# Kernel optimization log

Hardware: AMD Instinct MI355X
Metric: run time of the kernel (lower is better)

Reference implementation:

```python
import jax, jax.numpy as jnp
import numpy as np

IN_DIM = 4096
OUT_DIM = 2048
K = 4
R = 4096
B = 4096


def setup_inputs() -> dict:
    key = jax.random.key(0)
    ks = jax.random.split(key, 8)
    s = 0.02
    return {
        "hidden_states": jax.random.normal(ks[0], (B, IN_DIM), jnp.float32),
        # stacked per-block weights, torch Linear layout: W1/W3 [k+1, out, in], W2 [k+1, in, out]
        "W1": jax.random.normal(ks[1], (K + 1, OUT_DIM, IN_DIM), jnp.float32) * s,
        "W3": jax.random.normal(ks[2], (K + 1, OUT_DIM, IN_DIM), jnp.float32) * s,
        "W2": jax.random.normal(ks[3], (K + 1, IN_DIM, OUT_DIM), jnp.float32) * s,
        "fc1_w": jax.random.normal(ks[4], (R, IN_DIM * K), jnp.float32) * s,
        "fc1_b": jax.random.normal(ks[5], (R,), jnp.float32) * s,
        "fc2_w": jax.random.normal(ks[6], (IN_DIM, R), jnp.float32) * s,
        "fc2_b": jax.random.normal(ks[7], (IN_DIM,), jnp.float32) * s,
    }


def reference(hidden_states, W1, W3, W2, fc1_w, fc1_b, fc2_w, fc2_b):
    x = hidden_states
    # batched SwiGLU over k+1 blocks: [B, k+1, out]
    g = jax.nn.silu(jnp.einsum("bi,koi->bko", x, W1)) * jnp.einsum("bi,koi->bko", x, W3)
    wk_outs = jnp.einsum("bko,kio->bki", g, W2)  # [B, k+1, in]
    o0 = wk_outs[:, 0]                            # [B, in]
    concat = wk_outs[:, 1:].reshape(x.shape[0], -1)  # [B, k*in], matches torch.cat order
    h = jax.nn.silu(concat @ fc1_w.T + fc1_b)
    proj = h @ fc2_w.T + fc2_b                    # [B, in]
    diff = o0 - proj
    return (jnp.linalg.norm(diff, ord=2, axis=1), jnp.mean(jnp.abs(diff), axis=1))
```

## Files before the change

### kernel.cpp

```cpp
#include <hip/hip_runtime.h>
#include <hip/hip_bf16.h>
#include <cstdint>
#include <cstddef>

#define IN_DIM 4096
#define OUT_DIM 2048
#define NEXP 5
#define KEXP 4
#define RDIM 4096
#define BATCH 4096

typedef __hip_bfloat16 bf16;
typedef __attribute__((ext_vector_type(8))) short bf16x8;
typedef __attribute__((ext_vector_type(4))) float f32x4;
typedef __attribute__((ext_vector_type(8))) unsigned short u16x8;
typedef __attribute__((ext_vector_type(4))) unsigned short u16x4;

typedef const __attribute__((address_space(1))) unsigned int* as1p;
typedef __attribute__((address_space(3))) unsigned int* as3p;

__device__ __forceinline__ unsigned short f2bf(float x) {
  union { __hip_bfloat16 h; unsigned short u; } cv;
  cv.h = __float2bfloat16(x);
  return cv.u;
}

__global__ __launch_bounds__(256) void cvt_kernel(const float* __restrict__ in,
                                                  unsigned short* __restrict__ out,
                                                  int n8) {
  int i = blockIdx.x * 256 + threadIdx.x;
  if (i >= n8) return;
  const float4* p = (const float4*)in;
  float4 a = p[(size_t)i * 2];
  float4 b = p[(size_t)i * 2 + 1];
  u16x8 v;
  v[0] = f2bf(a.x); v[1] = f2bf(a.y); v[2] = f2bf(a.z); v[3] = f2bf(a.w);
  v[4] = f2bf(b.x); v[5] = f2bf(b.y); v[6] = f2bf(b.z); v[7] = f2bf(b.w);
  *(u16x8*)(out + (size_t)i * 8) = v;
}

__global__ __launch_bounds__(256) void tcvt_kernel(const float* __restrict__ in,
                                                   unsigned short* __restrict__ out,
                                                   int NI, int NO) {
  __shared__ float tile[32][33];
  const float* inz = in + (size_t)blockIdx.z * NI * NO;
  unsigned short* outz = out + (size_t)blockIdx.z * NI * NO;
  int i0 = blockIdx.y * 32;
  int o0 = blockIdx.x * 32;
  int t = threadIdx.x;
  int ri = t >> 3, ro = (t & 7) << 2;
  float4 v = *(const float4*)(inz + (size_t)(i0 + ri) * NO + o0 + ro);
  tile[ri][ro] = v.x; tile[ri][ro + 1] = v.y; tile[ri][ro + 2] = v.z; tile[ri][ro + 3] = v.w;
  __syncthreads();
  int wo = t >> 3, wi = (t & 7) << 2;
  u16x4 w;
  w[0] = f2bf(tile[wi][wo]);
  w[1] = f2bf(tile[wi + 1][wo]);
  w[2] = f2bf(tile[wi + 2][wo]);
  w[3] = f2bf(tile[wi + 3][wo]);
  *(u16x4*)(outz + (size_t)(o0 + wo) * NI + i0 + wi) = w;
}

__device__ __forceinline__ void gload16(const bf16* g, bf16* l) {
  __builtin_amdgcn_global_load_lds((as1p)g, (as3p)l, 16, 0, 0);
}

template <int N> __device__ __forceinline__ void vwait() {
  if constexpr (N == 0) asm volatile("s_waitcnt vmcnt(0)" ::: "memory");
  else if constexpr (N == 2) asm volatile("s_waitcnt vmcnt(2)" ::: "memory");
  else if constexpr (N == 4) asm volatile("s_waitcnt vmcnt(4)" ::: "memory");
}

#define READ_A(buf, mh)                                              \
  do {                                                               \
    const bf16* _pa = ldsA + (buf) * 16384 + (mh) * 8192;            \
    _Pragma("unroll") for (int m2 = 0; m2 < 4; ++m2) {               \
      afr[m2][0] = *(const bf16x8*)(_pa + aOff[m2]);                 \
      afr[m2][1] = *(const bf16x8*)(_pa + (aOff[m2] ^ 32));          \
    }                                                                \
  } while (0)

#define READ_B(buf, nh)                                              \
  do {                                                               \
    const bf16* _pb = ldsB + (buf) * 16384 + (nh) * 8192;            \
    _Pragma("unroll") for (int n2 = 0; n2 < 2; ++n2) {               \
      bfr[(nh) * 2 + n2][0] = *(const bf16x8*)(_pb + bOff[(nh) * 2 + n2]);        \
      bfr[(nh) * 2 + n2][1] = *(const bf16x8*)(_pb + (bOff[(nh) * 2 + n2] ^ 32)); \
    }                                                                \
  } while (0)

#define QMFMA(mh, nh)                                                            \
  do {                                                                           \
    __builtin_amdgcn_s_setprio(1);                                               \
    _Pragma("unroll") for (int m2 = 0; m2 < 4; ++m2) {                           \
      _Pragma("unroll") for (int n2 = 0; n2 < 2; ++n2) {                         \
        acc[(mh) * 4 + m2][(nh) * 2 + n2] = __builtin_amdgcn_mfma_f32_16x16x32_bf16( \
            afr[m2][0], bfr[(nh) * 2 + n2][0], acc[(mh) * 4 + m2][(nh) * 2 + n2], 0, 0, 0); \
        acc[(mh) * 4 + m2][(nh) * 2 + n2] = __builtin_amdgcn_mfma_f32_16x16x32_bf16( \
            afr[m2][1], bfr[(nh) * 2 + n2][1], acc[(mh) * 4 + m2][(nh) * 2 + n2], 0, 0, 0); \
      }                                                                          \
    }                                                                            \
    __builtin_amdgcn_s_setprio(0);                                               \
  } while (0)

#define BAR() __builtin_amdgcn_s_barrier()

template <int EPI>
__global__ __launch_bounds__(512, 2) void gemm8p(
    const bf16* __restrict__ A, int lda, long long aZ,
    const bf16* __restrict__ B, int ldb, long long bZ,
    int Kdim,
    unsigned short* __restrict__ C, int ldc, long long cZ,
    const float* __restrict__ bias,
    const bf16* __restrict__ AUX, int ldaux, long long auxZ,
    float* __restrict__ accum,
    int gx, int gxy, int nwg8) {
  extern __shared__ __align__(16) bf16 lds[];
  bf16* ldsA = lds;
  bf16* ldsB = lds + 32768;

  int flat = blockIdx.x;
  int wg = (flat & 7) * nwg8 + (flat >> 3);
  int z = wg / gxy;
  int r0 = wg - z * gxy;
  int by = r0 / gx;
  int bx = r0 - by * gx;
  int rowBase = by * 256, colBase = bx * 256;

  int tid = threadIdx.x;
  int wave = tid >> 6, lane = tid & 63;
  int wr = wave >> 2, wc = wave & 3;

  const bf16* Ab = A + (long long)z * aZ + (long long)rowBase * lda;
  const bf16* Bb = B + (long long)z * bZ + (long long)colBase * ldb;

  int rl = tid >> 3;
  int cg8 = ((tid & 7) ^ (rl & 7)) << 3;
  int srcA = rl * lda + cg8;
  int srcB = rl * ldb + cg8;
  int dstOfs = wave * 512;

  int aOff[4], bOff[4];
#pragma unroll
  for (int m2 = 0; m2 < 4; ++m2) {
    int rA = ((2 * m2 + wr) * 16) + (lane & 15);
    aOff[m2] = rA * 64 + (((lane >> 4) ^ (rA & 7)) << 3);
  }
#pragma unroll
  for (int n = 0; n < 4; ++n) {
    int rB = (((4 * n + wc) * 16) & 127) + (lane & 15);
    bOff[n] = rB * 64 + (((lane >> 4) ^ (rB & 7)) << 3);
  }

  f32x4 acc[8][4] = {};
  bf16x8 afr[4][2], bfr[4][2];

  auto stA = [&](int buf, int hh, int kt) {
    const bf16* s = Ab + (long long)(hh * 128) * lda + kt * 64;
    bf16* d = ldsA + buf * 16384 + hh * 8192 + dstOfs;
    gload16(s + srcA, d);
    gload16(s + srcA + 64 * lda, d + 4096);
  };
  auto stB = [&](int buf, int hh, int kt) {
    const bf16* s = Bb + (long long)(hh * 128) * ldb + kt * 64;
    bf16* d = ldsB + buf * 16384 + hh * 8192 + dstOfs;
    gload16(s + srcB, d);
    gload16(s + srcB + 64 * ldb, d + 4096);
  };

  int NT = Kdim >> 6;
  int cur = 0;

  stA(0, 0, 0); stB(0, 0, 0); stB(0, 1, 0); stA(0, 1, 0);
  vwait<4>();
  BAR();

  for (int t = 0; t < NT - 1; ++t) {
    int nb = cur ^ 1;
    READ_A(cur, 0);
    READ_B(cur, 0);
    stA(nb, 0, t + 1);
    vwait<4>();
    BAR();
    QMFMA(0, 0);
    READ_B(cur, 1);
    stB(nb, 0, t + 1);
    vwait<4>();
    BAR();
    QMFMA(0, 1);
    READ_A(cur, 1);
    stB(nb, 1, t + 1);
    BAR();
    QMFMA(1, 1);
    stA(nb, 1, t + 1);
    vwait<4>();
    BAR();
    QMFMA(1, 0);
    cur = nb;
  }

  READ_A(cur, 0);
  READ_B(cur, 0);
  vwait<2>();
  BAR();
  QMFMA(0, 0);
  READ_B(cur, 1);
  vwait<0>();
  BAR();
  QMFMA(0, 1);
  READ_A(cur, 1);
  QMFMA(1, 1);
  QMFMA(1, 0);

  if constexpr (EPI == 2) {
    const bf16* AUXb = AUX + (long long)z * auxZ;
#pragma unroll
    for (int m = 0; m < 8; ++m) {
#pragma unroll
      for (int r = 0; r < 4; ++r) {
        int row = rowBase + (2 * m + wr) * 16 + ((lane >> 4) << 2) + r;
        float ssq = 0.f, sab = 0.f;
#pragma unroll
        for (int n = 0; n < 4; ++n) {
          int col = colBase + (4 * n + wc) * 16 + (lane & 15);
          float p = acc[m][n][r] + bias[col];
          float d = __bfloat162float(AUXb[(long long)row * ldaux + col]) - p;
          ssq += d * d;
          sab += fabsf(d);
        }
#pragma unroll
        for (int off = 1; off < 16; off <<= 1) {
          ssq += __shfl_xor(ssq, off);
          sab += __shfl_xor(sab, off);
        }
        if ((lane & 15) == 0) {
          atomicAdd(&accum[row], ssq);
          atomicAdd(&accum[BATCH + row], sab);
        }
      }
    }
  } else {
    unsigned short* Cb = C + (long long)z * cZ;
    const bf16* AUXb = (EPI == 3) ? (AUX + (long long)z * auxZ) : nullptr;
#pragma unroll
    for (int m = 0; m < 8; ++m) {
#pragma unroll
      for (int n = 0; n < 4; ++n) {
        int col = colBase + (4 * n + wc) * 16 + (lane & 15);
#pragma unroll
        for (int r = 0; r < 4; ++r) {
          int row = rowBase + (2 * m + wr) * 16 + ((lane >> 4) << 2) + r;
          float v = acc[m][n][r];
          if constexpr (EPI == 1) {
            v += bias[col];
            v = v / (1.f + __expf(-v));
          } else if constexpr (EPI == 3) {
            float s = __bfloat162float(AUXb[(long long)row * ldaux + col]);
            v = v * (s / (1.f + __expf(-s)));
          }
          Cb[(long long)row * ldc + col] = f2bf(v);
        }
      }
    }
  }
}

#define READ_B1(buf)                                                  \
  do {                                                                \
    const bf16* _pb = ldsB1 + (buf) * 8192;                           \
    _Pragma("unroll") for (int n2 = 0; n2 < 2; ++n2) {                \
      b1fr[n2][0] = *(const bf16x8*)(_pb + bOff[n2]);                 \
      b1fr[n2][1] = *(const bf16x8*)(_pb + (bOff[n2] ^ 32));          \
    }                                                                 \
  } while (0)

#define READ_B3(buf)                                                  \
  do {                                                                \
    const bf16* _pb = ldsB3 + (buf) * 8192;                           \
    _Pragma("unroll") for (int n2 = 0; n2 < 2; ++n2) {                \
      b3fr[n2][0] = *(const bf16x8*)(_pb + bOff[n2]);                 \
      b3fr[n2][1] = *(const bf16x8*)(_pb + (bOff[n2] ^ 32));          \
    }                                                                 \
  } while (0)

#define QMFMA_D(ACC, mh, BF)                                                     \
  do {                                                                           \
    __builtin_amdgcn_s_setprio(1);                                               \
    _Pragma("unroll") for (int m2 = 0; m2 < 4; ++m2) {                           \
      _Pragma("unroll") for (int n2 = 0; n2 < 2; ++n2) {                         \
        ACC[(mh) * 4 + m2][n2] = __builtin_amdgcn_mfma_f32_16x16x32_bf16(        \
            afr[m2][0], BF[n2][0], ACC[(mh) * 4 + m2][n2], 0, 0, 0);             \
        ACC[(mh) * 4 + m2][n2] = __builtin_amdgcn_mfma_f32_16x16x32_bf16(        \
            afr[m2][1], BF[n2][1], ACC[(mh) * 4 + m2][n2], 0, 0, 0);             \
      }                                                                          \
    }                                                                            \
    __builtin_amdgcn_s_setprio(0);                                               \
  } while (0)

__global__ __launch_bounds__(512, 2) void gemm_dual(
    const bf16* __restrict__ A,
    const bf16* __restrict__ W1b, const bf16* __restrict__ W3b,
    unsigned short* __restrict__ G,
    int gx, int gxy, int nwg8) {
  extern __shared__ __align__(16) bf16 lds[];
  bf16* ldsA = lds;
  bf16* ldsB1 = lds + 32768;
  bf16* ldsB3 = lds + 49152;

  int flat = blockIdx.x;
  int wg = (flat & 7) * nwg8 + (flat >> 3);
  int z = wg / gxy;
  int r0 = wg - z * gxy;
  int by = r0 / gx;
  int bx = r0 - by * gx;
  int rowBase = by * 256, colBase = bx * 128;

  int tid = threadIdx.x;
  int wave = tid >> 6, lane = tid & 63;
  int wr = wave >> 2, wc = wave & 3;

  const bf16* Ab = A + (long long)rowBase * IN_DIM;
  const bf16* B1b = W1b + (long long)z * OUT_DIM * IN_DIM + (long long)colBase * IN_DIM;
  const bf16* B3b = W3b + (long long)z * OUT_DIM * IN_DIM + (long long)colBase * IN_DIM;

  int rl = tid >> 3;
  int cg8 = ((tid & 7) ^ (rl & 7)) << 3;
  int src = rl * IN_DIM + cg8;
  int dstOfs = wave * 512;

  int aOff[4], bOff[2];
#pragma unroll
  for (int m2 = 0; m2 < 4; ++m2) {
    int rA = ((2 * m2 + wr) * 16) + (lane & 15);
    aOff[m2] = rA * 64 + (((lane >> 4) ^ (rA & 7)) << 3);
  }
#pragma unroll
  for (int n2 = 0; n2 < 2; ++n2) {
    int rB = (4 * n2 + wc) * 16 + (lane & 15);
    bOff[n2] = rB * 64 + (((lane >> 4) ^ (rB & 7)) << 3);
  }

  f32x4 acc1[8][2] = {};
  f32x4 acc2[8][2] = {};
  bf16x8 afr[4][2], b1fr[2][2], b3fr[2][2];

  auto stA = [&](int buf, int hh, int kt) {
    const bf16* s = Ab + (long long)(hh * 128) * IN_DIM + kt * 64;
    bf16* d = ldsA + buf * 16384 + hh * 8192 + dstOfs;
    gload16(s + src, d);
    gload16(s + src + 64 * IN_DIM, d + 4096);
  };
  auto stB1 = [&](int buf, int kt) {
    const bf16* s = B1b + kt * 64;
    bf16* d = ldsB1 + buf * 8192 + dstOfs;
    gload16(s + src, d);
    gload16(s + src + 64 * IN_DIM, d + 4096);
  };
  auto stB3 = [&](int buf, int kt) {
    const bf16* s = B3b + kt * 64;
    bf16* d = ldsB3 + buf * 8192 + dstOfs;
    gload16(s + src, d);
    gload16(s + src + 64 * IN_DIM, d + 4096);
  };

  const int NT = IN_DIM >> 6;
  int cur = 0;

  stA(0, 0, 0); stB1(0, 0); stB3(0, 0); stA(0, 1, 0);
  vwait<4>();
  BAR();

  for (int t = 0; t < NT - 1; ++t) {
    int nb = cur ^ 1;
    READ_A(cur, 0);
    READ_B1(cur);
    stA(nb, 0, t + 1);
    vwait<4>();
    BAR();
    QMFMA_D(acc1, 0, b1fr);
    READ_B3(cur);
    stB1(nb, t + 1);
    vwait<4>();
    BAR();
    QMFMA_D(acc2, 0, b3fr);
    READ_A(cur, 1);
    stB3(nb, t + 1);
    BAR();
    QMFMA_D(acc1, 1, b1fr);
    stA(nb, 1, t + 1);
    vwait<4>();
    BAR();
    QMFMA_D(acc2, 1, b3fr);
    cur = nb;
  }

  READ_A(cur, 0);
  READ_B1(cur);
  vwait<2>();
  BAR();
  QMFMA_D(acc1, 0, b1fr);
  READ_B3(cur);
  vwait<0>();
  BAR();
  QMFMA_D(acc2, 0, b3fr);
  READ_A(cur, 1);
  QMFMA_D(acc1, 1, b1fr);
  QMFMA_D(acc2, 1, b3fr);

  unsigned short* Gb = G + (long long)z * OUT_DIM;
#pragma unroll
  for (int m = 0; m < 8; ++m) {
#pragma unroll
    for (int n2 = 0; n2 < 2; ++n2) {
      int col = colBase + (4 * n2 + wc) * 16 + (lane & 15);
#pragma unroll
      for (int r = 0; r < 4; ++r) {
        int row = rowBase + (2 * m + wr) * 16 + ((lane >> 4) << 2) + r;
        float v1 = acc1[m][n2][r], v2 = acc2[m][n2][r];
        float g = v2 * (v1 / (1.f + __expf(-v1)));
        Gb[(long long)row * (NEXP * OUT_DIM) + col] = f2bf(g);
      }
    }
  }
}

__global__ void zero_accum(float* a) {
  int i = blockIdx.x * 256 + threadIdx.x;
  if (i < 2 * BATCH) a[i] = 0.f;
}

__global__ void finalize_kernel(const float* __restrict__ accum, float* __restrict__ out) {
  int b = blockIdx.x * 256 + threadIdx.x;
  if (b < BATCH) {
    out[b] = sqrtf(accum[b]);
    out[BATCH + b] = accum[BATCH + b] * (1.f / IN_DIM);
  }
}

extern "C" void kernel_launch(void* const* d_in, const int* in_sizes, int n_in,
                              void* d_out, int out_size, void* d_ws, size_t ws_size,
                              hipStream_t stream) {
  const float* x    = (const float*)d_in[0];
  const float* W1   = (const float*)d_in[1];
  const float* W3   = (const float*)d_in[2];
  const float* W2   = (const float*)d_in[3];
  const float* fc1w = (const float*)d_in[4];
  const float* fc1b = (const float*)d_in[5];
  const float* fc2w = (const float*)d_in[6];
  const float* fc2b = (const float*)d_in[7];
  float* out = (float*)d_out;

  char* ws = (char*)d_ws;
  size_t off = 0;
  auto alloc = [&](size_t bytes) {
    char* p = ws + off;
    off += (bytes + 255) & ~(size_t)255;
    return p;
  };
  bf16* xb   = (bf16*)alloc((size_t)BATCH * IN_DIM * 2);
  bf16* w1b  = (bf16*)alloc((size_t)NEXP * OUT_DIM * IN_DIM * 2);
  bf16* w3b  = (bf16*)alloc((size_t)NEXP * OUT_DIM * IN_DIM * 2);
  bf16* w2b0 = (bf16*)alloc((size_t)IN_DIM * OUT_DIM * 2);
  bf16* w2t  = (bf16*)alloc((size_t)KEXP * OUT_DIM * IN_DIM * 2);
  bf16* f1b  = (bf16*)alloc((size_t)RDIM * IN_DIM * KEXP * 2);
  bf16* f2b  = (bf16*)alloc((size_t)IN_DIM * RDIM * 2);
  bf16* gbuf = (bf16*)alloc((size_t)BATCH * NEXP * OUT_DIM * 2);
  bf16* scratch = (bf16*)alloc((size_t)RDIM * KEXP * OUT_DIM * 2);
  bf16* o0   = (bf16*)alloc((size_t)BATCH * IN_DIM * 2);
  bf16* hbuf = (bf16*)alloc((size_t)BATCH * RDIM * 2);
  float* accum = (float*)alloc((size_t)2 * BATCH * 4);
  if (off > ws_size) return;

  bf16* Pcat = scratch;

  auto cvt = [&](const float* in, bf16* outp, size_t n) {
    int n8 = (int)(n / 8);
    cvt_kernel<<<(n8 + 255) / 256, 256, 0, stream>>>(in, (unsigned short*)outp, n8);
  };
  cvt(x,    xb,   (size_t)BATCH * IN_DIM);
  cvt(W1,   w1b,  (size_t)NEXP * OUT_DIM * IN_DIM);
  cvt(W3,   w3b,  (size_t)NEXP * OUT_DIM * IN_DIM);
  cvt(W2,   w2b0, (size_t)IN_DIM * OUT_DIM);
  cvt(fc1w, f1b,  (size_t)RDIM * IN_DIM * KEXP);
  cvt(fc2w, f2b,  (size_t)IN_DIM * RDIM);
  tcvt_kernel<<<dim3(OUT_DIM / 32, IN_DIM / 32, KEXP), 256, 0, stream>>>(
      W2 + (size_t)IN_DIM * OUT_DIM, (unsigned short*)w2t, IN_DIM, OUT_DIM);

  const size_t LDSB = 131072;

  {
    int gx = OUT_DIM / 128, gxy = gx * (BATCH / 256), nwg = gxy * NEXP;
    gemm_dual<<<nwg, 512, LDSB, stream>>>(
        xb, w1b, w3b, (unsigned short*)gbuf, gx, gxy, nwg / 8);
  }
  {
    int gx = IN_DIM / 256, gxy = gx * (BATCH / 256), nwg = gxy;
    gemm8p<0><<<nwg, 512, LDSB, stream>>>(
        gbuf, NEXP * OUT_DIM, 0LL,
        w2b0, OUT_DIM, 0LL,
        OUT_DIM,
        (unsigned short*)o0, IN_DIM, 0LL,
        nullptr, nullptr, 0, 0LL, nullptr,
        gx, gxy, nwg / 8);
  }
  {
    int gx = OUT_DIM / 256, gxy = gx * (RDIM / 256), nwg = gxy * KEXP;
    gemm8p<0><<<nwg, 512, LDSB, stream>>>(
        f1b, KEXP * IN_DIM, (long long)IN_DIM,
        w2t, IN_DIM, (long long)OUT_DIM * IN_DIM,
        IN_DIM,
        (unsigned short*)Pcat, KEXP * OUT_DIM, (long long)OUT_DIM,
        nullptr, nullptr, 0, 0LL, nullptr,
        gx, gxy, nwg / 8);
  }
  {
    int gx = RDIM / 256, gxy = gx * (BATCH / 256), nwg = gxy;
    gemm8p<1><<<nwg, 512, LDSB, stream>>>(
        gbuf + OUT_DIM, NEXP * OUT_DIM, 0LL,
        Pcat, KEXP * OUT_DIM, 0LL,
        KEXP * OUT_DIM,
        (unsigned short*)hbuf, RDIM, 0LL,
        fc1b, nullptr, 0, 0LL, nullptr,
        gx, gxy, nwg / 8);
  }
  zero_accum<<<(2 * BATCH + 255) / 256, 256, 0, stream>>>(accum);
  {
    int gx = IN_DIM / 256, gxy = gx * (BATCH / 256), nwg = gxy;
    gemm8p<2><<<nwg, 512, LDSB, stream>>>(
        hbuf, RDIM, 0LL,
        f2b, RDIM, 0LL,
        RDIM,
        nullptr, 0, 0LL,
        fc2b, o0, IN_DIM, 0LL, accum,
        gx, gxy, nwg / 8);
  }
  finalize_kernel<<<(BATCH + 255) / 256, 256, 0, stream>>>(accum, out);
}
```

Measured before the change: 1.374 ms.

## Fuse o0 GEMM into final GEMM via negated h and merge conversion launches

The separate o0 = g0 @ W2_0 GEMM is removed. The final kernel now runs two K-loops into one accumulator: g0·W2_0 plus hbuf·fc2_w, where hbuf holds the negated silu, so diff = acc - bias is formed directly. This avoids writing and re-reading the bf16 o0 buffer and its rounding step. It also merges the six fp32→bf16 conversion launches into one grid-stride kernel and moves zero_accum earlier.

```diff
diff --git a/kernel.cpp b/kernel.cpp
--- a/kernel.cpp
+++ b/kernel.cpp
@@ -25,18 +25,34 @@
   return cv.u;
 }
 
-__global__ __launch_bounds__(256) void cvt_kernel(const float* __restrict__ in,
-                                                  unsigned short* __restrict__ out,
-                                                  int n8) {
-  int i = blockIdx.x * 256 + threadIdx.x;
-  if (i >= n8) return;
-  const float4* p = (const float4*)in;
-  float4 a = p[(size_t)i * 2];
-  float4 b = p[(size_t)i * 2 + 1];
-  u16x8 v;
-  v[0] = f2bf(a.x); v[1] = f2bf(a.y); v[2] = f2bf(a.z); v[3] = f2bf(a.w);
-  v[4] = f2bf(b.x); v[5] = f2bf(b.y); v[6] = f2bf(b.z); v[7] = f2bf(b.w);
-  *(u16x8*)(out + (size_t)i * 8) = v;
+struct CvtArgs {
+  const float* src[6];
+  unsigned short* dst[6];
+  long long cum[6];
+};
+
+__global__ __launch_bounds__(256) void cvt_all_kernel(CvtArgs a, long long tot8) {
+  long long c0 = a.cum[0], c1 = a.cum[1], c2 = a.cum[2], c3 = a.cum[3], c4 = a.cum[4];
+  for (long long i = (long long)blockIdx.x * 256 + threadIdx.x; i < tot8;
+       i += (long long)gridDim.x * 256) {
+    int s = (int)(i >= c0) + (i >= c1) + (i >= c2) + (i >= c3) + (i >= c4);
+    const float* sp; unsigned short* dp; long long base;
+    switch (s) {
+      case 0: sp = a.src[0]; dp = a.dst[0]; base = 0;  break;
+      case 1: sp = a.src[1]; dp = a.dst[1]; base = c0; break;
+      case 2: sp = a.src[2]; dp = a.dst[2]; base = c1; break;
+      case 3: sp = a.src[3]; dp = a.dst[3]; base = c2; break;
+      case 4: sp = a.src[4]; dp = a.dst[4]; base = c3; break;
+      default: sp = a.src[5]; dp = a.dst[5]; base = c4; break;
+    }
+    long long j = i - base;
+    const float4* p = (const float4*)sp;
+    float4 va = p[j * 2], vb = p[j * 2 + 1];
+    u16x8 v;
+    v[0] = f2bf(va.x); v[1] = f2bf(va.y); v[2] = f2bf(va.z); v[3] = f2bf(va.w);
+    v[4] = f2bf(vb.x); v[5] = f2bf(vb.y); v[6] = f2bf(vb.z); v[7] = f2bf(vb.w);
+    *(u16x8*)(dp + j * 8) = v;
+  }
 }
 
 __global__ __launch_bounds__(256) void tcvt_kernel(const float* __restrict__ in,
@@ -110,9 +126,11 @@
     const bf16* __restrict__ A, int lda, long long aZ,
     const bf16* __restrict__ B, int ldb, long long bZ,
     int Kdim,
+    const bf16* __restrict__ A2, int lda2,
+    const bf16* __restrict__ B2, int ldb2,
+    int Kdim2,
     unsigned short* __restrict__ C, int ldc, long long cZ,
     const float* __restrict__ bias,
-    const bf16* __restrict__ AUX, int ldaux, long long auxZ,
     float* __restrict__ accum,
     int gx, int gxy, int nwg8) {
   extern __shared__ __align__(16) bf16 lds[];
@@ -131,13 +149,8 @@
   int wave = tid >> 6, lane = tid & 63;
   int wr = wave >> 2, wc = wave & 3;
 
-  const bf16* Ab = A + (long long)z * aZ + (long long)rowBase * lda;
-  const bf16* Bb = B + (long long)z * bZ + (long long)colBase * ldb;
-
   int rl = tid >> 3;
   int cg8 = ((tid & 7) ^ (rl & 7)) << 3;
-  int srcA = rl * lda + cg8;
-  int srcB = rl * ldb + cg8;
   int dstOfs = wave * 512;
 
   int aOff[4], bOff[4];
@@ -155,65 +168,76 @@
   f32x4 acc[8][4] = {};
   bf16x8 afr[4][2], bfr[4][2];
 
-  auto stA = [&](int buf, int hh, int kt) {
-    const bf16* s = Ab + (long long)(hh * 128) * lda + kt * 64;
-    bf16* d = ldsA + buf * 16384 + hh * 8192 + dstOfs;
-    gload16(s + srcA, d);
-    gload16(s + srcA + 64 * lda, d + 4096);
-  };
-  auto stB = [&](int buf, int hh, int kt) {
-    const bf16* s = Bb + (long long)(hh * 128) * ldb + kt * 64;
-    bf16* d = ldsB + buf * 16384 + hh * 8192 + dstOfs;
-    gload16(s + srcB, d);
-    gload16(s + srcB + 64 * ldb, d + 4096);
-  };
-
-  int NT = Kdim >> 6;
-  int cur = 0;
-
-  stA(0, 0, 0); stB(0, 0, 0); stB(0, 1, 0); stA(0, 1, 0);
-  vwait<4>();
-  BAR();
-
-  for (int t = 0; t < NT - 1; ++t) {
-    int nb = cur ^ 1;
+  auto runK = [&](const bf16* AbT, int lda_, const bf16* BbT, int ldb_, int NT) {
+    int srcA = rl * lda_ + cg8;
+    int srcB = rl * ldb_ + cg8;
+    auto stA = [&](int buf, int hh, int kt) {
+      const bf16* s = AbT + (long long)(hh * 128) * lda_ + kt * 64;
+      bf16* d = ldsA + buf * 16384 + hh * 8192 + dstOfs;
+      gload16(s + srcA, d);
+      gload16(s + srcA + 64 * lda_, d + 4096);
+    };
+    auto stB = [&](int buf, int hh, int kt) {
+      const bf16* s = BbT + (long long)(hh * 128) * ldb_ + kt * 64;
+      bf16* d = ldsB + buf * 16384 + hh * 8192 + dstOfs;
+      gload16(s + srcB, d);
+      gload16(s + srcB + 64 * ldb_, d + 4096);
+    };
+
+    int cur = 0;
+    stA(0, 0, 0); stB(0, 0, 0); stB(0, 1, 0); stA(0, 1, 0);
+    vwait<4>();
+    BAR();
+
+    for (int t = 0; t < NT - 1; ++t) {
+      int nb = cur ^ 1;
+      READ_A(cur, 0);
+      READ_B(cur, 0);
+      stA(nb, 0, t + 1);
+      vwait<4>();
+      BAR();
+      QMFMA(0, 0);
+      READ_B(cur, 1);
+      stB(nb, 0, t + 1);
+      vwait<4>();
+      BAR();
+      QMFMA(0, 1);
+      READ_A(cur, 1);
+      stB(nb, 1, t + 1);
+      BAR();
+      QMFMA(1, 1);
+      stA(nb, 1, t + 1);
+      vwait<4>();
+      BAR();
+      QMFMA(1, 0);
+      cur = nb;
+    }
+
     READ_A(cur, 0);
     READ_B(cur, 0);
-    stA(nb, 0, t + 1);
-    vwait<4>();
+    vwait<2>();
     BAR();
     QMFMA(0, 0);
     READ_B(cur, 1);
-    stB(nb, 0, t + 1);
-    vwait<4>();
+    vwait<0>();
     BAR();
     QMFMA(0, 1);
     READ_A(cur, 1);
-    stB(nb, 1, t + 1);
-    BAR();
     QMFMA(1, 1);
-    stA(nb, 1, t + 1);
-    vwait<4>();
-    BAR();
     QMFMA(1, 0);
-    cur = nb;
-  }
-
-  READ_A(cur, 0);
-  READ_B(cur, 0);
-  vwait<2>();
-  BAR();
-  QMFMA(0, 0);
-  READ_B(cur, 1);
-  vwait<0>();
-  BAR();
-  QMFMA(0, 1);
-  READ_A(cur, 1);
-  QMFMA(1, 1);
-  QMFMA(1, 0);
-
+    BAR();
+  };
+
+  runK(A + (long long)z * aZ + (long long)rowBase * lda, lda,
+       B + (long long)z * bZ + (long long)colBase * ldb, ldb,
+       Kdim >> 6);
   if constexpr (EPI == 2) {
-    const bf16* AUXb = AUX + (long long)z * auxZ;
+    runK(A2 + (long long)rowBase * lda2, lda2,
+         B2 + (long long)colBase * ldb2, ldb2,
+         Kdim2 >> 6);
+  }
+
+  if constexpr (EPI == 2) {
 #pragma unroll
     for (int m = 0; m < 8; ++m) {
 #pragma unroll
@@ -223,8 +247,7 @@
 #pragma unroll
         for (int n = 0; n < 4; ++n) {
           int col = colBase + (4 * n + wc) * 16 + (lane & 15);
-          float p = acc[m][n][r] + bias[col];
-          float d = __bfloat162float(AUXb[(long long)row * ldaux + col]) - p;
+          float d = acc[m][n][r] - bias[col];
           ssq += d * d;
           sab += fabsf(d);
         }
@@ -241,7 +264,6 @@
     }
   } else {
     unsigned short* Cb = C + (long long)z * cZ;
-    const bf16* AUXb = (EPI == 3) ? (AUX + (long long)z * auxZ) : nullptr;
 #pragma unroll
     for (int m = 0; m < 8; ++m) {
 #pragma unroll
@@ -253,10 +275,7 @@
           float v = acc[m][n][r];
           if constexpr (EPI == 1) {
             v += bias[col];
-            v = v / (1.f + __expf(-v));
-          } else if constexpr (EPI == 3) {
-            float s = __bfloat162float(AUXb[(long long)row * ldaux + col]);
-            v = v * (s / (1.f + __expf(-s)));
+            v = -(v / (1.f + __expf(-v)));
           }
           Cb[(long long)row * ldc + col] = f2bf(v);
         }
@@ -465,26 +484,34 @@
   bf16* f1b  = (bf16*)alloc((size_t)RDIM * IN_DIM * KEXP * 2);
   bf16* f2b  = (bf16*)alloc((size_t)IN_DIM * RDIM * 2);
   bf16* gbuf = (bf16*)alloc((size_t)BATCH * NEXP * OUT_DIM * 2);
-  bf16* scratch = (bf16*)alloc((size_t)RDIM * KEXP * OUT_DIM * 2);
-  bf16* o0   = (bf16*)alloc((size_t)BATCH * IN_DIM * 2);
+  bf16* Pcat = (bf16*)alloc((size_t)RDIM * KEXP * OUT_DIM * 2);
   bf16* hbuf = (bf16*)alloc((size_t)BATCH * RDIM * 2);
   float* accum = (float*)alloc((size_t)2 * BATCH * 4);
   if (off > ws_size) return;
 
-  bf16* Pcat = scratch;
-
-  auto cvt = [&](const float* in, bf16* outp, size_t n) {
-    int n8 = (int)(n / 8);
-    cvt_kernel<<<(n8 + 255) / 256, 256, 0, stream>>>(in, (unsigned short*)outp, n8);
-  };
-  cvt(x,    xb,   (size_t)BATCH * IN_DIM);
-  cvt(W1,   w1b,  (size_t)NEXP * OUT_DIM * IN_DIM);
-  cvt(W3,   w3b,  (size_t)NEXP * OUT_DIM * IN_DIM);
-  cvt(W2,   w2b0, (size_t)IN_DIM * OUT_DIM);
-  cvt(fc1w, f1b,  (size_t)RDIM * IN_DIM * KEXP);
-  cvt(fc2w, f2b,  (size_t)IN_DIM * RDIM);
+  {
+    CvtArgs a;
+    long long n8[6] = {
+        (long long)BATCH * IN_DIM / 8,
+        (long long)NEXP * OUT_DIM * IN_DIM / 8,
+        (long long)NEXP * OUT_DIM * IN_DIM / 8,
+        (long long)IN_DIM * OUT_DIM / 8,
+        (long long)RDIM * IN_DIM * KEXP / 8,
+        (long long)IN_DIM * RDIM / 8};
+    const float* srcs[6] = {x, W1, W3, W2, fc1w, fc2w};
+    unsigned short* dsts[6] = {(unsigned short*)xb, (unsigned short*)w1b,
+                               (unsigned short*)w3b, (unsigned short*)w2b0,
+                               (unsigned short*)f1b, (unsigned short*)f2b};
+    long long c = 0;
+    for (int i = 0; i < 6; ++i) {
+      a.src[i] = srcs[i]; a.dst[i] = dsts[i];
+      c += n8[i]; a.cum[i] = c;
+    }
+    cvt_all_kernel<<<2048, 256, 0, stream>>>(a, c);
+  }
   tcvt_kernel<<<dim3(OUT_DIM / 32, IN_DIM / 32, KEXP), 256, 0, stream>>>(
       W2 + (size_t)IN_DIM * OUT_DIM, (unsigned short*)w2t, IN_DIM, OUT_DIM);
+  zero_accum<<<(2 * BATCH + 255) / 256, 256, 0, stream>>>(accum);
 
   const size_t LDSB = 131072;
 
@@ -492,16 +519,6 @@
     int gx = OUT_DIM / 128, gxy = gx * (BATCH / 256), nwg = gxy * NEXP;
     gemm_dual<<<nwg, 512, LDSB, stream>>>(
         xb, w1b, w3b, (unsigned short*)gbuf, gx, gxy, nwg / 8);
-  }
-  {
-    int gx = IN_DIM / 256, gxy = gx * (BATCH / 256), nwg = gxy;
-    gemm8p<0><<<nwg, 512, LDSB, stream>>>(
-        gbuf, NEXP * OUT_DIM, 0LL,
-        w2b0, OUT_DIM, 0LL,
-        OUT_DIM,
-        (unsigned short*)o0, IN_DIM, 0LL,
-        nullptr, nullptr, 0, 0LL, nullptr,
-        gx, gxy, nwg / 8);
   }
   {
     int gx = OUT_DIM / 256, gxy = gx * (RDIM / 256), nwg = gxy * KEXP;
@@ -509,8 +526,9 @@
         f1b, KEXP * IN_DIM, (long long)IN_DIM,
         w2t, IN_DIM, (long long)OUT_DIM * IN_DIM,
         IN_DIM,
+        nullptr, 0, nullptr, 0, 0,
         (unsigned short*)Pcat, KEXP * OUT_DIM, (long long)OUT_DIM,
-        nullptr, nullptr, 0, 0LL, nullptr,
+        nullptr, nullptr,
         gx, gxy, nwg / 8);
   }
   {
@@ -519,19 +537,22 @@
         gbuf + OUT_DIM, NEXP * OUT_DIM, 0LL,
         Pcat, KEXP * OUT_DIM, 0LL,
         KEXP * OUT_DIM,
+        nullptr, 0, nullptr, 0, 0,
         (unsigned short*)hbuf, RDIM, 0LL,
-        fc1b, nullptr, 0, 0LL, nullptr,
+        fc1b, nullptr,
         gx, gxy, nwg / 8);
   }
-  zero_accum<<<(2 * BATCH + 255) / 256, 256, 0, stream>>>(accum);
   {
     int gx = IN_DIM / 256, gxy = gx * (BATCH / 256), nwg = gxy;
     gemm8p<2><<<nwg, 512, LDSB, stream>>>(
-        hbuf, RDIM, 0LL,
-        f2b, RDIM, 0LL,
+        gbuf, NEXP * OUT_DIM, 0LL,
+        w2b0, OUT_DIM, 0LL,
+        OUT_DIM,
+        hbuf, RDIM,
+        f2b, RDIM,
         RDIM,
         nullptr, 0, 0LL,
-        fc2b, o0, IN_DIM, 0LL, accum,
+        fc2b, accum,
         gx, gxy, nwg / 8);
   }
   finalize_kernel<<<(BATCH + 255) / 256, 256, 0, stream>>>(accum, out);
```

New measurement: 1.392 ms. About the same (+1.3%).
